# Kernel optimization log

Hardware: AMD Instinct MI355X
Metric: run time of the kernel (lower is better)

Reference implementation:

```python
import jax, jax.numpy as jnp
import numpy as np

B, M, IN, HID, A = 4096, 64, 3, 128, 64
D = 50.0                       # waveguide_bound
H_CONST = 5.0
PMAX = 10.0 ** (30 / 10 - 3)   # = 1.0 (30 dBm in Watts)
C_LIGHT = 3.0e8
FC = 6.0e9
DELTA_MIN = (C_LIGHT / FC) / 2.0  # 0.025
ALPHA = 0.2                    # LeakyReLU slope


def setup_inputs() -> dict:
    key = jax.random.key(0)
    ks = jax.random.split(key, 9)
    s = lambda k, sh: (jax.random.normal(k, sh, jnp.float32) * 0.1)
    return {
        "users": jax.random.normal(ks[0], (B, M, IN), jnp.float32),
        "W1": s(ks[1], (IN, HID)),    # GAT layer 1 projection (applied as h @ W)
        "a1": s(ks[2], (2 * HID,)),   # GAT layer 1 attention vector
        "W2": s(ks[3], (HID, HID)),   # GAT layer 2 projection
        "a2": s(ks[4], (2 * HID,)),
        "mw1": s(ks[5], (HID, 32)),   # MLP Linear(hidden, 32)
        "mb1": jnp.zeros((32,), jnp.float32),
        "mw2": s(ks[6], (32, 2 * A)), # MLP Linear(32, 2*num_antennas)
        "mb2": jnp.zeros((2 * A,), jnp.float32),
    }


def gat_layer(h, W, a):
    # Wh: [B, M, d]
    Wh = h @ W
    d = W.shape[1]
    # e[b,i,j] = leakyrelu( cat(Wh_i, Wh_j) . a ) = leakyrelu( Wh_i.a[:d] + Wh_j.a[d:] )
    si = Wh @ a[:d]          # [B, M]
    sj = Wh @ a[d:]          # [B, M]
    e = jax.nn.leaky_relu(si[:, :, None] + sj[:, None, :], ALPHA)  # [B, M, M]
    attn = jax.nn.softmax(e, axis=-1)  # softmax over neighbors j (dropout p=0 -> identity)
    h_prime = jnp.einsum('bij,bjd->bid', attn, Wh)
    return jax.nn.elu(h_prime)


def reference(users, W1, a1, W2, a2, mw1, mb1, mw2, mb2):
    h = gat_layer(users, W1, a1)
    h = gat_layer(h, W2, a2)
    pooled = jnp.max(h, axis=1)                      # [B, hidden]
    readout = jax.nn.relu(pooled @ mw1 + mb1) @ mw2 + mb2  # [B, 2A]
    raw_delta, raw_power = readout[:, :A], readout[:, A:]
    eps = 1e-6
    raw_delta = jax.nn.relu(raw_delta) + eps
    raw_power = jax.nn.relu(raw_power) + eps
    Bmax = 2.0 * D - (A - 1) * DELTA_MIN
    delta = Bmax * raw_delta / (jnp.sum(raw_delta, axis=1, keepdims=True) + eps)
    power = PMAX * raw_power / (jnp.sum(raw_power, axis=1, keepdims=True) + eps)
    return power, delta
```

## Files before the change

### kernel.cpp

```cpp
#include <hip/hip_runtime.h>

#define NBATCH 4096
#define OUT2 (NBATCH * 64)

typedef _Float16 f16;
typedef __attribute__((ext_vector_type(8))) _Float16 f16x8;
typedef __attribute__((ext_vector_type(4))) _Float16 f16x4;
typedef __attribute__((ext_vector_type(4))) float f32x4;

__device__ __forceinline__ float lrelu(float x) { return fmaxf(x, 0.2f * x); }
__device__ __forceinline__ float elu1(float x)  { return x > 0.0f ? x : __expf(x) - 1.0f; }

__global__ void prep(const float* __restrict__ W2, const float* __restrict__ W1,
                     const float* __restrict__ a1, const float* __restrict__ a2,
                     f16* __restrict__ w2b, float* __restrict__ w1a, f16* __restrict__ w2ab) {
    const int flat = blockIdx.x * 256 + threadIdx.x;
    const int slot = flat >> 3, j = flat & 7;
    const int F2T = slot >> 8, kf = (slot >> 6) & 3, ln = slot & 63;
    const int lq = ln >> 4, lr = ln & 15;
    w2b[flat] = (f16)W2[(kf * 32 + lq * 8 + j) * 128 + F2T * 16 + lr];
    if (flat < 2048) {
        const int ks = flat >> 9, ln2 = (flat >> 3) & 63, jj = flat & 7;
        const int k = ks * 32 + ((ln2 >> 4) & 3) * 8 + jj;
        const int n = ln2 & 15;
        float v = 0.f;
        if (n < 2) {
            const float* av = a2 + n * 128;
            for (int f2 = 0; f2 < 128; ++f2) v = fmaf(W2[k * 128 + f2], av[f2], v);
        }
        w2ab[flat] = (f16)v;
    }
    if (flat >= 16381) {
        const int c = flat - 16381;
        float si = 0.f, sj = 0.f;
        for (int f = 0; f < 128; ++f) {
            const float w = W1[c * 128 + f];
            si = fmaf(w, a1[f], si);
            sj = fmaf(w, a1[128 + f], sj);
        }
        w1a[c] = si; w1a[3 + c] = sj;
    }
}

__global__ __launch_bounds__(64, 2)
void gat_kernel(const float* __restrict__ users,
                const float* __restrict__ W1,
                const f16* __restrict__ w2b,
                const float* __restrict__ w1a,
                const f16* __restrict__ w2ab,
                const float* __restrict__ mw1,
                const float* __restrict__ mb1,
                const float* __restrict__ mw2,
                const float* __restrict__ mb2,
                float* __restrict__ out)
{
    const int b = blockIdx.x;
    const int lane = threadIdx.x;
    const int lr = lane & 15;
    const int lq = lane >> 4;

    __shared__ __align__(16) char smem[9344];
    f16*   sMain = (f16*)smem;
    float* sSi   = (float*)(smem + 8192);
    float* sSj   = (float*)(smem + 8448);
    float* sPool = (float*)(smem + 8704);
    float* sHid  = (float*)(smem + 9216);

    const float* u = users + b * 192;

    {
        const float x = u[lane * 3], y = u[lane * 3 + 1], z = u[lane * 3 + 2];
        sSi[lane] = fmaf(x, w1a[0], fmaf(y, w1a[1], z * w1a[2]));
        sSj[lane] = fmaf(x, w1a[3], fmaf(y, w1a[4], z * w1a[5]));
    }
    __syncthreads();

    f16x8 bfr[4];
    {
        float sjv[16];
        *(float4*)&sjv[0]  = *(const float4*)&sSj[lq * 8];
        *(float4*)&sjv[4]  = *(const float4*)&sSj[lq * 8 + 4];
        *(float4*)&sjv[8]  = *(const float4*)&sSj[32 + lq * 8];
        *(float4*)&sjv[12] = *(const float4*)&sSj[32 + lq * 8 + 4];
        f16x8 ap[4][2];
        #pragma unroll
        for (int mt = 0; mt < 4; ++mt) {
            const float si = sSi[mt * 16 + lr];
            float pv[16];
            float lsum = 0.f;
            #pragma unroll
            for (int jj = 0; jj < 8; ++jj) {
                const float t0 = si + sjv[jj];
                const float t1 = si + sjv[8 + jj];
                const float p0 = __expf(lrelu(t0));
                const float p1 = __expf(lrelu(t1));
                pv[jj] = p0; pv[8 + jj] = p1;
                lsum += p0 + p1;
            }
            lsum += __shfl_xor(lsum, 16, 64);
            lsum += __shfl_xor(lsum, 32, 64);
            const float inv = 1.0f / lsum;
            #pragma unroll
            for (int jj = 0; jj < 8; ++jj) {
                ap[mt][0][jj] = (f16)(pv[jj] * inv);
                ap[mt][1][jj] = (f16)(pv[8 + jj] * inv);
            }
        }
        f16x8 af2[2];
        #pragma unroll
        for (int ks = 0; ks < 2; ++ks) {
            #pragma unroll
            for (int jj = 0; jj < 8; ++jj) {
                const int node = ks * 32 + lq * 8 + jj;
                af2[ks][jj] = (lr < 3) ? (f16)u[node * 3 + lr] : (f16)0.f;
            }
        }
        #pragma unroll
        for (int nt = 0; nt < 4; ++nt) {
            f32x4 d1 = (f32x4){0.f, 0.f, 0.f, 0.f};
            d1 = __builtin_amdgcn_mfma_f32_16x16x32_f16(af2[0], ap[nt][0], d1, 0, 0, 0);
            d1 = __builtin_amdgcn_mfma_f32_16x16x32_f16(af2[1], ap[nt][1], d1, 0, 0, 0);
            const float c0 = __shfl(d1[0], lr, 64);
            const float c1 = __shfl(d1[1], lr, 64);
            const float c2 = __shfl(d1[2], lr, 64);
            #pragma unroll
            for (int jj = 0; jj < 8; ++jj) bfr[nt][jj] = (f16)0.f;
            if (lq == 0) {
                bfr[nt][0] = (f16)c0; bfr[nt][1] = (f16)c1; bfr[nt][2] = (f16)c2;
            }
        }
    }

    f16x8 hf[4][4];
    #pragma unroll
    for (int h = 0; h < 2; ++h) {
        __syncthreads();
        #pragma unroll
        for (int ftl = 0; ftl < 4; ++ftl) {
            f16x8 af3;
            #pragma unroll
            for (int jj = 0; jj < 8; ++jj) af3[jj] = (f16)0.f;
            if (lq == 0) {
                #pragma unroll
                for (int jj = 0; jj < 3; ++jj)
                    af3[jj] = (f16)W1[jj * 128 + (h * 4 + ftl) * 16 + lr];
            }
            #pragma unroll
            for (int nt = 0; nt < 4; ++nt) {
                f32x4 acc = (f32x4){0.f, 0.f, 0.f, 0.f};
                acc = __builtin_amdgcn_mfma_f32_16x16x32_f16(af3, bfr[nt], acc, 0, 0, 0);
                f16x4 hv;
                #pragma unroll
                for (int r = 0; r < 4; ++r) hv[r] = (f16)elu1(acc[r]);
                const int n = nt * 16 + lr;
                const int gg = 2 * ftl + (lq >> 1);
                *(f16x4*)&sMain[n * 64 + ((gg ^ (n & 7)) << 3) + ((lq & 1) * 4)] = hv;
            }
        }
        __syncthreads();
        #pragma unroll
        for (int nt = 0; nt < 4; ++nt) {
            const int n = nt * 16 + lr;
            #pragma unroll
            for (int ksl = 0; ksl < 2; ++ksl)
                hf[nt][h * 2 + ksl] =
                    *(const f16x8*)&sMain[n * 64 + (((ksl * 4 + lq) ^ (n & 7)) << 3)];
        }
    }

    {
        f32x4 sacc[4];
        #pragma unroll
        for (int mt = 0; mt < 4; ++mt) sacc[mt] = (f32x4){0.f, 0.f, 0.f, 0.f};
        #pragma unroll
        for (int ks = 0; ks < 4; ++ks) {
            f16x8 bsw = *(const f16x8*)(w2ab + (ks * 64 + lane) * 8);
            #pragma unroll
            for (int mt = 0; mt < 4; ++mt)
                sacc[mt] = __builtin_amdgcn_mfma_f32_16x16x32_f16(hf[mt][ks], bsw, sacc[mt], 0, 0, 0);
        }
        __syncthreads();
        if (lr < 2) {
            float* dst = (lr == 0) ? sSi : sSj;
            #pragma unroll
            for (int mt = 0; mt < 4; ++mt)
                #pragma unroll
                for (int r = 0; r < 4; ++r)
                    dst[mt * 16 + lq * 4 + r] = sacc[mt][r];
        }
    }
    __syncthreads();

    f16x8 bp[4][2];
    {
        float sjv[16];
        *(float4*)&sjv[0]  = *(const float4*)&sSj[lq * 8];
        *(float4*)&sjv[4]  = *(const float4*)&sSj[lq * 8 + 4];
        *(float4*)&sjv[8]  = *(const float4*)&sSj[32 + lq * 8];
        *(float4*)&sjv[12] = *(const float4*)&sSj[32 + lq * 8 + 4];
        #pragma unroll
        for (int mt = 0; mt < 4; ++mt) {
            const float si = sSi[mt * 16 + lr];
            float pv[16];
            float lsum = 0.f;
            #pragma unroll
            for (int jj = 0; jj < 8; ++jj) {
                const float t0 = si + sjv[jj];
                const float t1 = si + sjv[8 + jj];
                const float p0 = __expf(lrelu(t0));
                const float p1 = __expf(lrelu(t1));
                pv[jj] = p0; pv[8 + jj] = p1;
                lsum += p0 + p1;
            }
            lsum += __shfl_xor(lsum, 16, 64);
            lsum += __shfl_xor(lsum, 32, 64);
            const float inv = 1.0f / lsum;
            #pragma unroll
            for (int jj = 0; jj < 8; ++jj) {
                bp[mt][0][jj] = (f16)(pv[jj] * inv);
                bp[mt][1][jj] = (f16)(pv[8 + jj] * inv);
            }
        }
    }

    int fst[4];
    #pragma unroll
    for (int nt = 0; nt < 4; ++nt) {
        const int gg = nt * 2 + (lq >> 1);
        fst[nt] = lr * 64 + ((gg ^ (lr & 7)) << 3) + ((lq & 1) * 4);
    }
    const int er0 = lr * 64 + ((lq ^ (lr & 7)) << 3);
    const int er1 = lr * 64 + (((4 + lq) ^ (lr & 7)) << 3);

    {
        f16x8 bw2[4];
        #pragma unroll
        for (int kf = 0; kf < 4; ++kf)
            bw2[kf] = *(const f16x8*)(w2b + ((0 * 4 + kf) * 64 + lane) * 8);
        #pragma unroll
        for (int nt = 0; nt < 4; ++nt) {
            f32x4 acc = (f32x4){0.f, 0.f, 0.f, 0.f};
            #pragma unroll
            for (int kf = 0; kf < 4; ++kf)
                acc = __builtin_amdgcn_mfma_f32_16x16x32_f16(hf[nt][kf], bw2[kf], acc, 0, 0, 0);
            f16x4 hv;
            #pragma unroll
            for (int r = 0; r < 4; ++r) hv[r] = (f16)acc[r];
            *(f16x4*)&sMain[fst[nt]] = hv;
        }
    }
    __syncthreads();

    #pragma unroll 1
    for (int ft = 0; ft < 8; ++ft) {
        f16* rb = sMain + ((ft & 1) << 10);
        if (ft < 7) {
            f16* wb = sMain + (((ft + 1) & 1) << 10);
            f16x8 bw2[4];
            #pragma unroll
            for (int kf = 0; kf < 4; ++kf)
                bw2[kf] = *(const f16x8*)(w2b + (((ft + 1) * 4 + kf) * 64 + lane) * 8);
            #pragma unroll
            for (int nt = 0; nt < 4; ++nt) {
                f32x4 acc = (f32x4){0.f, 0.f, 0.f, 0.f};
                #pragma unroll
                for (int kf = 0; kf < 4; ++kf)
                    acc = __builtin_amdgcn_mfma_f32_16x16x32_f16(hf[nt][kf], bw2[kf], acc, 0, 0, 0);
                f16x4 hv;
                #pragma unroll
                for (int r = 0; r < 4; ++r) hv[r] = (f16)acc[r];
                *(f16x4*)&wb[fst[nt]] = hv;
            }
        }

        f16x8 bh0 = *(const f16x8*)&rb[er0];
        f16x8 bh1 = *(const f16x8*)&rb[er1];
        float mx = -1e30f;
        #pragma unroll
        for (int mt = 0; mt < 4; ++mt) {
            f32x4 acc = (f32x4){0.f, 0.f, 0.f, 0.f};
            acc = __builtin_amdgcn_mfma_f32_16x16x32_f16(bp[mt][0], bh0, acc, 0, 0, 0);
            acc = __builtin_amdgcn_mfma_f32_16x16x32_f16(bp[mt][1], bh1, acc, 0, 0, 0);
            mx = fmaxf(mx, fmaxf(fmaxf(acc[0], acc[1]), fmaxf(acc[2], acc[3])));
        }
        mx = fmaxf(mx, __shfl_xor(mx, 16, 64));
        mx = fmaxf(mx, __shfl_xor(mx, 32, 64));
        if (lane < 16) sPool[ft * 16 + lane] = elu1(mx);
        __syncthreads();
    }

    {
        const int o = lane & 31, hh = lane >> 5;
        float s0 = 0.f;
        #pragma unroll 8
        for (int kk = 0; kk < 64; ++kk) {
            const int c = hh * 64 + kk;
            s0 = fmaf(sPool[c], mw1[c * 32 + o], s0);
        }
        s0 += __shfl_xor(s0, 32, 64);
        if (lane < 32) sHid[lane] = fmaxf(s0 + mb1[o], 0.0f);
    }
    __syncthreads();
    {
        float sA = mb2[lane], sB = mb2[64 + lane];
        #pragma unroll 8
        for (int q = 0; q < 32; ++q) {
            const float wA = mw2[q * 128 + lane];
            const float wB = mw2[q * 128 + 64 + lane];
            const float h0 = sHid[q];
            sA = fmaf(h0, wA, sA);  sB = fmaf(h0, wB, sB);
        }
        float rA = fmaxf(sA, 0.0f) + 1e-6f, rB = fmaxf(sB, 0.0f) + 1e-6f;
        float uA = rA, uB = rB;
        #pragma unroll
        for (int m = 1; m < 64; m <<= 1) {
            uA += __shfl_xor(uA, m, 64);  uB += __shfl_xor(uB, m, 64);
        }
        out[b * 64 + lane]        = rB / (uB + 1e-6f);
        out[OUT2 + b * 64 + lane] = 98.425f * rA / (uA + 1e-6f);
    }
}

extern "C" void kernel_launch(void* const* d_in, const int* in_sizes, int n_in,
                              void* d_out, int out_size, void* d_ws, size_t ws_size,
                              hipStream_t stream) {
    const float* users = (const float*)d_in[0];
    const float* W1    = (const float*)d_in[1];
    const float* a1    = (const float*)d_in[2];
    const float* W2    = (const float*)d_in[3];
    const float* a2    = (const float*)d_in[4];
    const float* mw1   = (const float*)d_in[5];
    const float* mb1   = (const float*)d_in[6];
    const float* mw2   = (const float*)d_in[7];
    const float* mb2   = (const float*)d_in[8];
    float* out = (float*)d_out;

    f16*   w2b  = (f16*)d_ws;
    float* w1a  = (float*)((char*)d_ws + 32768);
    f16*   w2ab = (f16*)((char*)d_ws + 32800);

    prep<<<64, 256, 0, stream>>>(W2, W1, a1, a2, w2b, w1a, w2ab);
    gat_kernel<<<NBATCH, 64, 0, stream>>>(users, W1, w2b, w1a, w2ab,
                                          mw1, mb1, mw2, mb2, out);
}
```

Measured before the change: 114.9 us.

## Split each batch element across two wavefronts by node tiles

The GAT kernel now runs two wavefronts per batch element, each owning two of the four 16-node tiles through attention, projection and aggregation. The partial max-pools are combined through shared memory, and the readout halves are split between the waves. Softmax exponentials are recomputed rather than stored to lower register pressure. The aim is more parallel waves and lower per-wave latency, at the cost of extra shared-memory traffic and the duplicated exp work.

```diff
diff --git a/kernel.cpp b/kernel.cpp
--- a/kernel.cpp
+++ b/kernel.cpp
@@ -42,7 +42,7 @@
     }
 }
 
-__global__ __launch_bounds__(64, 2)
+__global__ __launch_bounds__(128, 2)
 void gat_kernel(const float* __restrict__ users,
                 const float* __restrict__ W1,
                 const f16* __restrict__ w2b,
@@ -54,56 +54,52 @@
                 const float* __restrict__ mb2,
                 float* __restrict__ out)
 {
-    const int b = blockIdx.x;
-    const int lane = threadIdx.x;
-    const int lr = lane & 15;
-    const int lq = lane >> 4;
-
-    __shared__ __align__(16) char smem[9344];
+    const int b    = blockIdx.x;
+    const int tid  = threadIdx.x;
+    const int wid  = tid >> 6;
+    const int lane = tid & 63;
+    const int lr   = lane & 15;
+    const int lq   = lane >> 4;
+    const int mtb  = wid * 2;
+
+    __shared__ __align__(16) char smem[9856];
     f16*   sMain = (f16*)smem;
     float* sSi   = (float*)(smem + 8192);
     float* sSj   = (float*)(smem + 8448);
-    float* sPool = (float*)(smem + 8704);
-    float* sHid  = (float*)(smem + 9216);
+    float* sPH   = (float*)(smem + 8704);
+    float* sHid  = (float*)(smem + 9728);
 
     const float* u = users + b * 192;
 
     {
         const float x = u[lane * 3], y = u[lane * 3 + 1], z = u[lane * 3 + 2];
-        sSi[lane] = fmaf(x, w1a[0], fmaf(y, w1a[1], z * w1a[2]));
-        sSj[lane] = fmaf(x, w1a[3], fmaf(y, w1a[4], z * w1a[5]));
-    }
-    __syncthreads();
-
-    f16x8 bfr[4];
+        if (wid == 0) sSi[lane] = fmaf(x, w1a[0], fmaf(y, w1a[1], z * w1a[2]));
+        else          sSj[lane] = fmaf(x, w1a[3], fmaf(y, w1a[4], z * w1a[5]));
+    }
+    __syncthreads();
+
+    f16x8 bfr[2];
     {
         float sjv[16];
         *(float4*)&sjv[0]  = *(const float4*)&sSj[lq * 8];
         *(float4*)&sjv[4]  = *(const float4*)&sSj[lq * 8 + 4];
         *(float4*)&sjv[8]  = *(const float4*)&sSj[32 + lq * 8];
         *(float4*)&sjv[12] = *(const float4*)&sSj[32 + lq * 8 + 4];
-        f16x8 ap[4][2];
-        #pragma unroll
-        for (int mt = 0; mt < 4; ++mt) {
-            const float si = sSi[mt * 16 + lr];
-            float pv[16];
+        f16x8 ap[2][2];
+        #pragma unroll
+        for (int m = 0; m < 2; ++m) {
+            const float si = sSi[(mtb + m) * 16 + lr];
             float lsum = 0.f;
             #pragma unroll
-            for (int jj = 0; jj < 8; ++jj) {
-                const float t0 = si + sjv[jj];
-                const float t1 = si + sjv[8 + jj];
-                const float p0 = __expf(lrelu(t0));
-                const float p1 = __expf(lrelu(t1));
-                pv[jj] = p0; pv[8 + jj] = p1;
-                lsum += p0 + p1;
-            }
+            for (int jj = 0; jj < 8; ++jj)
+                lsum += __expf(lrelu(si + sjv[jj])) + __expf(lrelu(si + sjv[8 + jj]));
             lsum += __shfl_xor(lsum, 16, 64);
             lsum += __shfl_xor(lsum, 32, 64);
             const float inv = 1.0f / lsum;
             #pragma unroll
             for (int jj = 0; jj < 8; ++jj) {
-                ap[mt][0][jj] = (f16)(pv[jj] * inv);
-                ap[mt][1][jj] = (f16)(pv[8 + jj] * inv);
+                ap[m][0][jj] = (f16)(__expf(lrelu(si + sjv[jj])) * inv);
+                ap[m][1][jj] = (f16)(__expf(lrelu(si + sjv[8 + jj])) * inv);
             }
         }
         f16x8 af2[2];
@@ -116,25 +112,24 @@
             }
         }
         #pragma unroll
-        for (int nt = 0; nt < 4; ++nt) {
+        for (int m = 0; m < 2; ++m) {
             f32x4 d1 = (f32x4){0.f, 0.f, 0.f, 0.f};
-            d1 = __builtin_amdgcn_mfma_f32_16x16x32_f16(af2[0], ap[nt][0], d1, 0, 0, 0);
-            d1 = __builtin_amdgcn_mfma_f32_16x16x32_f16(af2[1], ap[nt][1], d1, 0, 0, 0);
+            d1 = __builtin_amdgcn_mfma_f32_16x16x32_f16(af2[0], ap[m][0], d1, 0, 0, 0);
+            d1 = __builtin_amdgcn_mfma_f32_16x16x32_f16(af2[1], ap[m][1], d1, 0, 0, 0);
             const float c0 = __shfl(d1[0], lr, 64);
             const float c1 = __shfl(d1[1], lr, 64);
             const float c2 = __shfl(d1[2], lr, 64);
             #pragma unroll
-            for (int jj = 0; jj < 8; ++jj) bfr[nt][jj] = (f16)0.f;
+            for (int jj = 0; jj < 8; ++jj) bfr[m][jj] = (f16)0.f;
             if (lq == 0) {
-                bfr[nt][0] = (f16)c0; bfr[nt][1] = (f16)c1; bfr[nt][2] = (f16)c2;
-            }
-        }
-    }
-
-    f16x8 hf[4][4];
+                bfr[m][0] = (f16)c0; bfr[m][1] = (f16)c1; bfr[m][2] = (f16)c2;
+            }
+        }
+    }
+
+    f16x8 hf[2][4];
     #pragma unroll
     for (int h = 0; h < 2; ++h) {
-        __syncthreads();
         #pragma unroll
         for (int ftl = 0; ftl < 4; ++ftl) {
             f16x8 af3;
@@ -146,52 +141,53 @@
                     af3[jj] = (f16)W1[jj * 128 + (h * 4 + ftl) * 16 + lr];
             }
             #pragma unroll
-            for (int nt = 0; nt < 4; ++nt) {
+            for (int m = 0; m < 2; ++m) {
                 f32x4 acc = (f32x4){0.f, 0.f, 0.f, 0.f};
-                acc = __builtin_amdgcn_mfma_f32_16x16x32_f16(af3, bfr[nt], acc, 0, 0, 0);
+                acc = __builtin_amdgcn_mfma_f32_16x16x32_f16(af3, bfr[m], acc, 0, 0, 0);
                 f16x4 hv;
                 #pragma unroll
                 for (int r = 0; r < 4; ++r) hv[r] = (f16)elu1(acc[r]);
-                const int n = nt * 16 + lr;
+                const int n = (mtb + m) * 16 + lr;
                 const int gg = 2 * ftl + (lq >> 1);
                 *(f16x4*)&sMain[n * 64 + ((gg ^ (n & 7)) << 3) + ((lq & 1) * 4)] = hv;
             }
         }
-        __syncthreads();
-        #pragma unroll
-        for (int nt = 0; nt < 4; ++nt) {
-            const int n = nt * 16 + lr;
+        asm volatile("s_waitcnt lgkmcnt(0)" ::: "memory");
+        #pragma unroll
+        for (int m = 0; m < 2; ++m) {
+            const int n = (mtb + m) * 16 + lr;
             #pragma unroll
             for (int ksl = 0; ksl < 2; ++ksl)
-                hf[nt][h * 2 + ksl] =
+                hf[m][h * 2 + ksl] =
                     *(const f16x8*)&sMain[n * 64 + (((ksl * 4 + lq) ^ (n & 7)) << 3)];
         }
-    }
-
-    {
-        f32x4 sacc[4];
-        #pragma unroll
-        for (int mt = 0; mt < 4; ++mt) sacc[mt] = (f32x4){0.f, 0.f, 0.f, 0.f};
+        asm volatile("s_waitcnt lgkmcnt(0)" ::: "memory");
+    }
+
+    {
+        f32x4 sacc[2];
+        #pragma unroll
+        for (int m = 0; m < 2; ++m) sacc[m] = (f32x4){0.f, 0.f, 0.f, 0.f};
         #pragma unroll
         for (int ks = 0; ks < 4; ++ks) {
             f16x8 bsw = *(const f16x8*)(w2ab + (ks * 64 + lane) * 8);
             #pragma unroll
-            for (int mt = 0; mt < 4; ++mt)
-                sacc[mt] = __builtin_amdgcn_mfma_f32_16x16x32_f16(hf[mt][ks], bsw, sacc[mt], 0, 0, 0);
+            for (int m = 0; m < 2; ++m)
+                sacc[m] = __builtin_amdgcn_mfma_f32_16x16x32_f16(hf[m][ks], bsw, sacc[m], 0, 0, 0);
         }
         __syncthreads();
         if (lr < 2) {
             float* dst = (lr == 0) ? sSi : sSj;
             #pragma unroll
-            for (int mt = 0; mt < 4; ++mt)
+            for (int m = 0; m < 2; ++m)
                 #pragma unroll
                 for (int r = 0; r < 4; ++r)
-                    dst[mt * 16 + lq * 4 + r] = sacc[mt][r];
-        }
-    }
-    __syncthreads();
-
-    f16x8 bp[4][2];
+                    dst[(mtb + m) * 16 + lq * 4 + r] = sacc[m][r];
+        }
+    }
+    __syncthreads();
+
+    f16x8 bp[2][2];
     {
         float sjv[16];
         *(float4*)&sjv[0]  = *(const float4*)&sSj[lq * 8];
@@ -199,35 +195,28 @@
         *(float4*)&sjv[8]  = *(const float4*)&sSj[32 + lq * 8];
         *(float4*)&sjv[12] = *(const float4*)&sSj[32 + lq * 8 + 4];
         #pragma unroll
-        for (int mt = 0; mt < 4; ++mt) {
-            const float si = sSi[mt * 16 + lr];
-            float pv[16];
+        for (int m = 0; m < 2; ++m) {
+            const float si = sSi[(mtb + m) * 16 + lr];
             float lsum = 0.f;
             #pragma unroll
-            for (int jj = 0; jj < 8; ++jj) {
-                const float t0 = si + sjv[jj];
-                const float t1 = si + sjv[8 + jj];
-                const float p0 = __expf(lrelu(t0));
-                const float p1 = __expf(lrelu(t1));
-                pv[jj] = p0; pv[8 + jj] = p1;
-                lsum += p0 + p1;
-            }
+            for (int jj = 0; jj < 8; ++jj)
+                lsum += __expf(lrelu(si + sjv[jj])) + __expf(lrelu(si + sjv[8 + jj]));
             lsum += __shfl_xor(lsum, 16, 64);
             lsum += __shfl_xor(lsum, 32, 64);
             const float inv = 1.0f / lsum;
             #pragma unroll
             for (int jj = 0; jj < 8; ++jj) {
-                bp[mt][0][jj] = (f16)(pv[jj] * inv);
-                bp[mt][1][jj] = (f16)(pv[8 + jj] * inv);
-            }
-        }
-    }
-
-    int fst[4];
+                bp[m][0][jj] = (f16)(__expf(lrelu(si + sjv[jj])) * inv);
+                bp[m][1][jj] = (f16)(__expf(lrelu(si + sjv[8 + jj])) * inv);
+            }
+        }
+    }
+
+    int fst[2];
     #pragma unroll
-    for (int nt = 0; nt < 4; ++nt) {
-        const int gg = nt * 2 + (lq >> 1);
-        fst[nt] = lr * 64 + ((gg ^ (lr & 7)) << 3) + ((lq & 1) * 4);
+    for (int m = 0; m < 2; ++m) {
+        const int gg = (mtb + m) * 2 + (lq >> 1);
+        fst[m] = lr * 64 + ((gg ^ (lr & 7)) << 3) + ((lq & 1) * 4);
     }
     const int er0 = lr * 64 + ((lq ^ (lr & 7)) << 3);
     const int er1 = lr * 64 + (((4 + lq) ^ (lr & 7)) << 3);
@@ -238,15 +227,15 @@
         for (int kf = 0; kf < 4; ++kf)
             bw2[kf] = *(const f16x8*)(w2b + ((0 * 4 + kf) * 64 + lane) * 8);
         #pragma unroll
-        for (int nt = 0; nt < 4; ++nt) {
+        for (int m = 0; m < 2; ++m) {
             f32x4 acc = (f32x4){0.f, 0.f, 0.f, 0.f};
             #pragma unroll
             for (int kf = 0; kf < 4; ++kf)
-                acc = __builtin_amdgcn_mfma_f32_16x16x32_f16(hf[nt][kf], bw2[kf], acc, 0, 0, 0);
+                acc = __builtin_amdgcn_mfma_f32_16x16x32_f16(hf[m][kf], bw2[kf], acc, 0, 0, 0);
             f16x4 hv;
             #pragma unroll
             for (int r = 0; r < 4; ++r) hv[r] = (f16)acc[r];
-            *(f16x4*)&sMain[fst[nt]] = hv;
+            *(f16x4*)&sMain[fst[m]] = hv;
         }
     }
     __syncthreads();
@@ -261,15 +250,15 @@
             for (int kf = 0; kf < 4; ++kf)
                 bw2[kf] = *(const f16x8*)(w2b + (((ft + 1) * 4 + kf) * 64 + lane) * 8);
             #pragma unroll
-            for (int nt = 0; nt < 4; ++nt) {
+            for (int m = 0; m < 2; ++m) {
                 f32x4 acc = (f32x4){0.f, 0.f, 0.f, 0.f};
                 #pragma unroll
                 for (int kf = 0; kf < 4; ++kf)
-                    acc = __builtin_amdgcn_mfma_f32_16x16x32_f16(hf[nt][kf], bw2[kf], acc, 0, 0, 0);
+                    acc = __builtin_amdgcn_mfma_f32_16x16x32_f16(hf[m][kf], bw2[kf], acc, 0, 0, 0);
                 f16x4 hv;
                 #pragma unroll
                 for (int r = 0; r < 4; ++r) hv[r] = (f16)acc[r];
-                *(f16x4*)&wb[fst[nt]] = hv;
+                *(f16x4*)&wb[fst[m]] = hv;
             }
         }
 
@@ -277,47 +266,48 @@
         f16x8 bh1 = *(const f16x8*)&rb[er1];
         float mx = -1e30f;
         #pragma unroll
-        for (int mt = 0; mt < 4; ++mt) {
+        for (int m = 0; m < 2; ++m) {
             f32x4 acc = (f32x4){0.f, 0.f, 0.f, 0.f};
-            acc = __builtin_amdgcn_mfma_f32_16x16x32_f16(bp[mt][0], bh0, acc, 0, 0, 0);
-            acc = __builtin_amdgcn_mfma_f32_16x16x32_f16(bp[mt][1], bh1, acc, 0, 0, 0);
+            acc = __builtin_amdgcn_mfma_f32_16x16x32_f16(bp[m][0], bh0, acc, 0, 0, 0);
+            acc = __builtin_amdgcn_mfma_f32_16x16x32_f16(bp[m][1], bh1, acc, 0, 0, 0);
             mx = fmaxf(mx, fmaxf(fmaxf(acc[0], acc[1]), fmaxf(acc[2], acc[3])));
         }
         mx = fmaxf(mx, __shfl_xor(mx, 16, 64));
         mx = fmaxf(mx, __shfl_xor(mx, 32, 64));
-        if (lane < 16) sPool[ft * 16 + lane] = elu1(mx);
+        if (lane < 16) sPH[wid * 128 + ft * 16 + lane] = mx;
         __syncthreads();
     }
 
     {
+        const float v = elu1(fmaxf(sPH[tid], sPH[128 + tid]));
+        sPH[tid] = v;
+    }
+    __syncthreads();
+
+    if (wid == 0) {
         const int o = lane & 31, hh = lane >> 5;
         float s0 = 0.f;
         #pragma unroll 8
         for (int kk = 0; kk < 64; ++kk) {
             const int c = hh * 64 + kk;
-            s0 = fmaf(sPool[c], mw1[c * 32 + o], s0);
+            s0 = fmaf(sPH[c], mw1[c * 32 + o], s0);
         }
         s0 += __shfl_xor(s0, 32, 64);
         if (lane < 32) sHid[lane] = fmaxf(s0 + mb1[o], 0.0f);
     }
     __syncthreads();
     {
-        float sA = mb2[lane], sB = mb2[64 + lane];
+        const int cbase = (wid == 0) ? 64 : 0;
+        float s = mb2[cbase + lane];
         #pragma unroll 8
-        for (int q = 0; q < 32; ++q) {
-            const float wA = mw2[q * 128 + lane];
-            const float wB = mw2[q * 128 + 64 + lane];
-            const float h0 = sHid[q];
-            sA = fmaf(h0, wA, sA);  sB = fmaf(h0, wB, sB);
-        }
-        float rA = fmaxf(sA, 0.0f) + 1e-6f, rB = fmaxf(sB, 0.0f) + 1e-6f;
-        float uA = rA, uB = rB;
-        #pragma unroll
-        for (int m = 1; m < 64; m <<= 1) {
-            uA += __shfl_xor(uA, m, 64);  uB += __shfl_xor(uB, m, 64);
-        }
-        out[b * 64 + lane]        = rB / (uB + 1e-6f);
-        out[OUT2 + b * 64 + lane] = 98.425f * rA / (uA + 1e-6f);
+        for (int q = 0; q < 32; ++q)
+            s = fmaf(sHid[q], mw2[q * 128 + cbase + lane], s);
+        float r = fmaxf(s, 0.0f) + 1e-6f;
+        float uu = r;
+        #pragma unroll
+        for (int m = 1; m < 64; m <<= 1) uu += __shfl_xor(uu, m, 64);
+        if (wid == 0) out[b * 64 + lane]        = r / (uu + 1e-6f);
+        else          out[OUT2 + b * 64 + lane] = 98.425f * r / (uu + 1e-6f);
     }
 }
 
@@ -340,6 +330,6 @@
     f16*   w2ab = (f16*)((char*)d_ws + 32800);
 
     prep<<<64, 256, 0, stream>>>(W2, W1, a1, a2, w2b, w1a, w2ab);
-    gat_kernel<<<NBATCH, 64, 0, stream>>>(users, W1, w2b, w1a, w2ab,
-                                          mw1, mb1, mw2, mb2, out);
+    gat_kernel<<<NBATCH, 128, 0, stream>>>(users, W1, w2b, w1a, w2ab,
+                                           mw1, mb1, mw2, mb2, out);
 }
```

Result: slower. 118.3 us (+3.0%).

## Pack four batch items per workgroup and use wave-local LDS fences

Applied to the files above, without the earlier changes.

Each 256-thread workgroup now runs four independent single-wave batch items, each with its own slice of shared memory. The launch uses a quarter as many workgroups. Because every wave touches only its own LDS slice, the workgroup barriers are replaced with `s_waitcnt lgkmcnt(0)` fences, which cuts dispatch overhead and barrier cost. This relies on in-order LDS handling within a wave for correctness, and the larger per-workgroup LDS footprint and changed launch bounds may alter occupancy and register allocation.

```diff
diff --git a/kernel.cpp b/kernel.cpp
--- a/kernel.cpp
+++ b/kernel.cpp
@@ -10,6 +10,9 @@
 
 __device__ __forceinline__ float lrelu(float x) { return fmaxf(x, 0.2f * x); }
 __device__ __forceinline__ float elu1(float x)  { return x > 0.0f ? x : __expf(x) - 1.0f; }
+__device__ __forceinline__ void lds_fence() {
+    asm volatile("s_waitcnt lgkmcnt(0)" ::: "memory");
+}
 
 __global__ void prep(const float* __restrict__ W2, const float* __restrict__ W1,
                      const float* __restrict__ a1, const float* __restrict__ a2,
@@ -42,7 +45,7 @@
     }
 }
 
-__global__ __launch_bounds__(64, 2)
+__global__ __launch_bounds__(256, 2)
 void gat_kernel(const float* __restrict__ users,
                 const float* __restrict__ W1,
                 const f16* __restrict__ w2b,
@@ -54,17 +57,19 @@
                 const float* __restrict__ mb2,
                 float* __restrict__ out)
 {
-    const int b = blockIdx.x;
-    const int lane = threadIdx.x;
-    const int lr = lane & 15;
-    const int lq = lane >> 4;
-
-    __shared__ __align__(16) char smem[9344];
-    f16*   sMain = (f16*)smem;
-    float* sSi   = (float*)(smem + 8192);
-    float* sSj   = (float*)(smem + 8448);
-    float* sPool = (float*)(smem + 8704);
-    float* sHid  = (float*)(smem + 9216);
+    const int wid  = threadIdx.x >> 6;
+    const int b    = blockIdx.x * 4 + wid;
+    const int lane = threadIdx.x & 63;
+    const int lr   = lane & 15;
+    const int lq   = lane >> 4;
+
+    __shared__ __align__(16) char smem[4 * 9344];
+    char*  sw    = smem + wid * 9344;
+    f16*   sMain = (f16*)sw;
+    float* sSi   = (float*)(sw + 8192);
+    float* sSj   = (float*)(sw + 8448);
+    float* sPool = (float*)(sw + 8704);
+    float* sHid  = (float*)(sw + 9216);
 
     const float* u = users + b * 192;
 
@@ -73,7 +78,7 @@
         sSi[lane] = fmaf(x, w1a[0], fmaf(y, w1a[1], z * w1a[2]));
         sSj[lane] = fmaf(x, w1a[3], fmaf(y, w1a[4], z * w1a[5]));
     }
-    __syncthreads();
+    lds_fence();
 
     f16x8 bfr[4];
     {
@@ -134,7 +139,6 @@
     f16x8 hf[4][4];
     #pragma unroll
     for (int h = 0; h < 2; ++h) {
-        __syncthreads();
         #pragma unroll
         for (int ftl = 0; ftl < 4; ++ftl) {
             f16x8 af3;
@@ -157,7 +161,7 @@
                 *(f16x4*)&sMain[n * 64 + ((gg ^ (n & 7)) << 3) + ((lq & 1) * 4)] = hv;
             }
         }
-        __syncthreads();
+        lds_fence();
         #pragma unroll
         for (int nt = 0; nt < 4; ++nt) {
             const int n = nt * 16 + lr;
@@ -166,6 +170,7 @@
                 hf[nt][h * 2 + ksl] =
                     *(const f16x8*)&sMain[n * 64 + (((ksl * 4 + lq) ^ (n & 7)) << 3)];
         }
+        lds_fence();
     }
 
     {
@@ -179,7 +184,6 @@
             for (int mt = 0; mt < 4; ++mt)
                 sacc[mt] = __builtin_amdgcn_mfma_f32_16x16x32_f16(hf[mt][ks], bsw, sacc[mt], 0, 0, 0);
         }
-        __syncthreads();
         if (lr < 2) {
             float* dst = (lr == 0) ? sSi : sSj;
             #pragma unroll
@@ -189,7 +193,7 @@
                     dst[mt * 16 + lq * 4 + r] = sacc[mt][r];
         }
     }
-    __syncthreads();
+    lds_fence();
 
     f16x8 bp[4][2];
     {
@@ -249,7 +253,7 @@
             *(f16x4*)&sMain[fst[nt]] = hv;
         }
     }
-    __syncthreads();
+    lds_fence();
 
     #pragma unroll 1
     for (int ft = 0; ft < 8; ++ft) {
@@ -286,7 +290,7 @@
         mx = fmaxf(mx, __shfl_xor(mx, 16, 64));
         mx = fmaxf(mx, __shfl_xor(mx, 32, 64));
         if (lane < 16) sPool[ft * 16 + lane] = elu1(mx);
-        __syncthreads();
+        lds_fence();
     }
 
     {
@@ -300,7 +304,7 @@
         s0 += __shfl_xor(s0, 32, 64);
         if (lane < 32) sHid[lane] = fmaxf(s0 + mb1[o], 0.0f);
     }
-    __syncthreads();
+    lds_fence();
     {
         float sA = mb2[lane], sB = mb2[64 + lane];
         #pragma unroll 8
@@ -340,6 +344,6 @@
     f16*   w2ab = (f16*)((char*)d_ws + 32800);
 
     prep<<<64, 256, 0, stream>>>(W2, W1, a1, a2, w2b, w1a, w2ab);
-    gat_kernel<<<NBATCH, 64, 0, stream>>>(users, W1, w2b, w1a, w2ab,
-                                          mw1, mb1, mw2, mb2, out);
+    gat_kernel<<<NBATCH / 4, 256, 0, stream>>>(users, W1, w2b, w1a, w2ab,
+                                               mw1, mb1, mw2, mb2, out);
 }
```

Measured after the change: 114.7 us. No clear change (-0.2%).
